# Kernel optimization log

Hardware: AMD Instinct MI355X
Metric: run time of the kernel (lower is better)

## Reference

```python
import jax, jax.numpy as jnp
import numpy as np

TEMPERATURE = 0.07
EPS = 1e-8

def setup_inputs() -> dict:
    key = jax.random.key(0)
    k1, k2 = jax.random.split(key)
    features = jax.random.normal(k1, (8192, 512), dtype=jnp.float32)
    labels = jax.random.randint(k2, (8192,), 0, 100, dtype=jnp.int64)
    return {"features": features, "labels": labels}

def reference(features, labels):
    # L2-normalize rows (torch F.normalize uses eps=1e-12 clamp on norm)
    norm = jnp.maximum(jnp.linalg.norm(features, axis=1, keepdims=True), 1e-12)
    f = features / norm                                   # [B, D]
    sim = jnp.matmul(f, f.T) / TEMPERATURE                # [B, B]
    B = features.shape[0]
    same_label = (labels[:, None] == labels[None, :]).astype(features.dtype)
    diag = jnp.eye(B, dtype=bool)
    mask = jnp.where(diag, 0.0, same_label)               # positives, diag removed
    exp_sim = jnp.where(diag, 0.0, jnp.exp(sim))          # diag zeroed
    positive_sum = jnp.sum(exp_sim * mask, axis=1)        # [B]
    negative_sum = jnp.sum(exp_sim * (1.0 - mask), axis=1)
    loss = -jnp.log(positive_sum / (positive_sum + negative_sum + EPS))
    return loss.mean()
```

## Files before the change

kernel.cpp:

```cpp
#include <hip/hip_runtime.h>

#define BATCH 8192
#define DIM   512
#define NBLK  1056

typedef __attribute__((ext_vector_type(2))) long long2_t;
typedef __attribute__((ext_vector_type(4))) float f32x4;
typedef unsigned short ushort_t;
typedef unsigned char  u8;

__device__ __forceinline__ void gload_lds16(const void* g, void* l){
  __builtin_amdgcn_global_load_lds(
      (const __attribute__((address_space(1))) void*)g,
      (__attribute__((address_space(3))) void*)l, 16, 0, 0);
}

template<int CTRL>
__device__ __forceinline__ float dpp_add(float v){
  int s = __builtin_amdgcn_update_dpp(0, __float_as_int(v), CTRL, 0xF, 0xF, true);
  return v + __int_as_float(s);
}
__device__ __forceinline__ float red16(float v){
  v = dpp_add<0xB1>(v);
  v = dpp_add<0x4E>(v);
  v = dpp_add<0x141>(v);
  v = dpp_add<0x140>(v);
  return v;
}

__device__ __forceinline__ u8 f2e4m3(float v){
  unsigned s = (__float_as_uint(v) >> 24) & 0x80u;
  float a = fabsf(v);
  if (a < 0.0009765625f) return (u8)s;
  if (a < 0.015625f){
    int q = (int)rintf(a * 512.0f);
    return (u8)(s | (unsigned)q);
  }
  unsigned u = __float_as_uint(a);
  int E = (int)(u >> 23) - 127;
  unsigned m = u & 0x7FFFFF;
  unsigned mant = m >> 20;
  unsigned rem  = m & 0xFFFFF;
  mant += (rem > 0x80000u || (rem == 0x80000u && (mant & 1u))) ? 1u : 0u;
  if (mant == 8u){ mant = 0u; E += 1; }
  return (u8)(s | ((unsigned)(E + 7) << 3) | mant);
}

__global__ __launch_bounds__(256) void k_normalize(const float* __restrict__ x,
                                                   u8* __restrict__ q){
  const int row  = blockIdx.x * 4 + (threadIdx.x >> 6);
  const int lane = threadIdx.x & 63;
  const float* xr = x + (size_t)row * DIM + lane * 8;
  float4 a = *(const float4*)xr;
  float4 b = *(const float4*)(xr + 4);
  float s = a.x*a.x + a.y*a.y + a.z*a.z + a.w*a.w
          + b.x*b.x + b.y*b.y + b.z*b.z + b.w*b.w;
  #pragma unroll
  for (int m = 1; m < 64; m <<= 1) s += __shfl_xor(s, m);
  const float inv = 1.0f / fmaxf(sqrtf(s), 1e-12f);
  float f[8] = {a.x, a.y, a.z, a.w, b.x, b.y, b.z, b.w};
  union { u8 b[8]; unsigned long long u; } pk;
  #pragma unroll
  for (int e = 0; e < 8; e++) pk.b[e] = f2e4m3(f[e] * inv);
  const int kb = lane >> 3;
  const int g  = lane & 7;
  const int sw = (row >> 1) & 3;
  const size_t off = (size_t)row * DIM + kb * 64
                   + (size_t)(((g & 3) ^ sw) * 16 + (g >> 2) * 8);
  *(unsigned long long*)(q + off) = pk.u;
}

__global__ __launch_bounds__(256, 2) void k_gemm(const u8* __restrict__ q,
                                                 const int* __restrict__ labels,
                                                 float* __restrict__ ppos,
                                                 float* __restrict__ ptot){
  __shared__ u8 sA[2][256 * 64];
  __shared__ u8 sB[2][128 * 64];
  __shared__ int labI[256], labJ[128];

  const int bid = (blockIdx.x & 7) * 132 + (blockIdx.x >> 3);
  int I = (int)((65.0f - sqrtf(4225.0f - 4.0f * (float)bid)) * 0.5f);
  while ((I + 1) * (64 - I) <= bid) I++;
  while (I * (65 - I) > bid) I--;
  const int J = 2 * I + (bid - I * (65 - I));
  const bool mirror = (J >= 2 * I + 2);
  const int rowbase = I * 256, colbase = J * 128;

  const int t    = threadIdx.x;
  const int lane = t & 63;
  const int w    = t >> 6;
  const int wr   = w >> 1, wc = w & 1;
  const int lrow = lane & 15;
  const int g    = lane >> 4;

  labI[t] = labels[rowbase + t];
  if (t < 128) labJ[t] = labels[colbase + t];

  const int gs = (g ^ ((lrow >> 1) & 3)) * 16;
  int ra[8], rb[4];
  #pragma unroll
  for (int m = 0; m < 8; m++) ra[m] = (wr * 128 + m * 16 + lrow) * 64 + gs;
  #pragma unroll
  for (int n = 0; n < 4; n++) rb[n] = (wc * 64 + n * 16 + lrow) * 64 + gs;

  const u8* srcA = q + (size_t)(rowbase + (t >> 2)) * DIM + (t & 3) * 16;
  const u8* srcB = q + (size_t)(colbase + (t >> 2)) * DIM + (t & 3) * 16;
  const int dL = t * 16;

#define STAGE(BUF, KT) do{                                                \
    gload_lds16(srcA + (KT) * 64,                  sA[BUF] + dL);         \
    gload_lds16(srcA + (KT) * 64 +  64 * DIM,      sA[BUF] + dL + 4096);  \
    gload_lds16(srcA + (KT) * 64 + 128 * DIM,      sA[BUF] + dL + 8192);  \
    gload_lds16(srcA + (KT) * 64 + 192 * DIM,      sA[BUF] + dL + 12288); \
    gload_lds16(srcB + (KT) * 64,                  sB[BUF] + dL);         \
    gload_lds16(srcB + (KT) * 64 +  64 * DIM,      sB[BUF] + dL + 4096);  \
  }while(0)

  f32x4 acc[8][4];
  #pragma unroll
  for (int m = 0; m < 8; m++)
    #pragma unroll
    for (int n = 0; n < 4; n++)
      acc[m][n] = (f32x4){0.f, 0.f, 0.f, 0.f};

  STAGE(0, 0);
  __syncthreads();

  for (int kt = 0; kt < 8; ++kt){
    const int cur = kt & 1;
    if (kt < 7) STAGE(cur ^ 1, kt + 1);
    const u8* pA = sA[cur];
    const u8* pB = sB[cur];
    long2_t av[8], bv[4];
    #pragma unroll
    for (int n = 0; n < 4; n++) bv[n] = *(const long2_t*)(pB + rb[n]);
    #pragma unroll
    for (int m = 0; m < 8; m++) av[m] = *(const long2_t*)(pA + ra[m]);
    #pragma unroll
    for (int m = 0; m < 8; m++)
      #pragma unroll
      for (int n = 0; n < 4; n++)
        acc[m][n] = __builtin_amdgcn_mfma_f32_16x16x32_fp8_fp8(
            av[m][0], bv[n][0], acc[m][n], 0, 0, 0);
    #pragma unroll
    for (int m = 0; m < 8; m++)
      #pragma unroll
      for (int n = 0; n < 4; n++)
        acc[m][n] = __builtin_amdgcn_mfma_f32_16x16x32_fp8_fp8(
            av[m][1], bv[n][1], acc[m][n], 0, 0, 0);
    __syncthreads();
  }
#undef STAGE

  const int i0 = rowbase + wr * 128;
  const int j0 = colbase + wc * 64;

  int li_[8][4], lj_[4];
  #pragma unroll
  for (int m = 0; m < 8; m++)
    #pragma unroll
    for (int e = 0; e < 4; e++)
      li_[m][e] = labI[wr * 128 + m * 16 + g * 4 + e];
  #pragma unroll
  for (int n = 0; n < 4; n++)
    lj_[n] = labJ[wc * 64 + n * 16 + lrow];

  const float invT = 14.285714285714286f;
  #pragma unroll
  for (int m = 0; m < 8; m++)
    #pragma unroll
    for (int n = 0; n < 4; n++)
      #pragma unroll
      for (int e = 0; e < 4; e++){
        int i = i0 + m * 16 + g * 4 + e;
        int j = j0 + n * 16 + lrow;
        acc[m][n][e] = (i == j) ? 0.0f : __expf(acc[m][n][e] * invT);
      }

  {
    float* pp = ppos + (size_t)(J * 2 + wc) * BATCH;
    float* pt = ptot + (size_t)(J * 2 + wc) * BATCH;
    #pragma unroll
    for (int m = 0; m < 8; m++){
      float tr[4] = {0, 0, 0, 0}, pr[4] = {0, 0, 0, 0};
      #pragma unroll
      for (int n = 0; n < 4; n++){
        int lj = lj_[n];
        #pragma unroll
        for (int e = 0; e < 4; e++){
          float v = acc[m][n][e];
          tr[e] += v;
          pr[e] += (li_[m][e] == lj) ? v : 0.0f;
        }
      }
      #pragma unroll
      for (int e = 0; e < 4; e++){
        tr[e] = red16(tr[e]);
        pr[e] = red16(pr[e]);
      }
      if (lrow == 0){
        int ib = i0 + m * 16 + g * 4;
        #pragma unroll
        for (int e = 0; e < 4; e++){
          pt[ib + e] = tr[e];
          pp[ib + e] = pr[e];
        }
      }
    }
  }

  if (mirror){
    #pragma unroll
    for (int h = 0; h < 2; h++){
      float* pp = ppos + (size_t)(I * 4 + wr * 2 + h) * BATCH;
      float* pt = ptot + (size_t)(I * 4 + wr * 2 + h) * BATCH;
      #pragma unroll
      for (int n = 0; n < 4; n++){
        float ts = 0.f, ps = 0.f;
        int lj = lj_[n];
        #pragma unroll
        for (int m = h * 4; m < h * 4 + 4; m++)
          #pragma unroll
          for (int e = 0; e < 4; e++){
            float v = acc[m][n][e];
            ts += v;
            ps += (li_[m][e] == lj) ? v : 0.0f;
          }
        ts += __shfl_xor(ts, 16); ps += __shfl_xor(ps, 16);
        ts += __shfl_xor(ts, 32); ps += __shfl_xor(ps, 32);
        if (lane < 16){
          int j = j0 + n * 16 + lane;
          pt[j] = ts;
          pp[j] = ps;
        }
      }
    }
  }
}

__global__ __launch_bounds__(256) void k_rowloss(const float* __restrict__ ppos,
                                                 const float* __restrict__ ptot,
                                                 float* __restrict__ bsum){
  __shared__ float sp[256], st2[256];
  const int t = threadIdx.x;
  const int r = blockIdx.x * 32 + (t & 31);
  const int c0 = t >> 5;
  float p = 0.f, tt = 0.f;
  for (int c = c0; c < 128; c += 8){
    p  += ppos[(size_t)c * BATCH + r];
    tt += ptot[(size_t)c * BATCH + r];
  }
  sp[t] = p; st2[t] = tt;
  __syncthreads();
  if (t < 32){
    float P = 0.f, T = 0.f;
    #pragma unroll
    for (int k = 0; k < 8; k++){ P += sp[t + k * 32]; T += st2[t + k * 32]; }
    sp[t] = -logf(P / (T + 1e-8f));
  }
  __syncthreads();
  if (t == 0){
    float s = 0.f;
    #pragma unroll
    for (int k = 0; k < 32; k++) s += sp[k];
    bsum[blockIdx.x] = s;
  }
}

__global__ __launch_bounds__(256) void k_final(const float* __restrict__ bsum,
                                               float* __restrict__ out){
  __shared__ float s4[4];
  float v = bsum[threadIdx.x];
  #pragma unroll
  for (int m = 1; m < 64; m <<= 1) v += __shfl_xor(v, m);
  if ((threadIdx.x & 63) == 0) s4[threadIdx.x >> 6] = v;
  __syncthreads();
  if (threadIdx.x == 0) out[0] = (s4[0] + s4[1] + s4[2] + s4[3]) * (1.0f / 8192.0f);
}

extern "C" void kernel_launch(void* const* d_in, const int* in_sizes, int n_in,
                              void* d_out, int out_size, void* d_ws, size_t ws_size,
                              hipStream_t stream){
  const float* x      = (const float*)d_in[0];
  const int*   labels = (const int*)d_in[1];
  float*       out    = (float*)d_out;

  char* ws = (char*)d_ws;
  u8*    q    = (u8*)ws;
  float* ppos = (float*)(ws + 8388608);
  float* ptot = (float*)(ws + 8388608 + 4194304);
  float* bsum = (float*)(ws + 8388608 + 8388608);

  k_normalize<<<BATCH / 4, 256, 0, stream>>>(x, q);
  k_gemm<<<NBLK, 256, 0, stream>>>(q, labels, ppos, ptot);
  k_rowloss<<<256, 256, 0, stream>>>(ppos, ptot, bsum);
  k_final<<<1, 256, 0, stream>>>(bsum, out);
}
```

Before: 59.55 us.

## Shrink GEMM tile to 128x128 over upper-triangular blocks with higher occupancy

Changes the symmetric Gram-matrix tiling from 256x128 tiles over a 2-column-wide triangular layout to square 128x128 tiles indexed over the upper triangle, giving 2080 blocks instead of 1056. Per-thread accumulators shrink from 8x4 to 4x4 MFMA tiles and LDS use drops, so launch bounds move to 3 blocks per CU. The aim is better load balance and occupancy across the CUs. In exchange, operand reuse per tile is lower, global/LDS traffic rises and more partial sums are written. It also passes a dynamic shared memory argument of 8192 bytes that the kernel does not appear to use.

```diff
diff --git a/kernel.cpp b/kernel.cpp
--- a/kernel.cpp
+++ b/kernel.cpp
@@ -2,12 +2,11 @@
 
 #define BATCH 8192
 #define DIM   512
-#define NBLK  1056
+#define NBLK  2080
 
 typedef __attribute__((ext_vector_type(2))) long long2_t;
 typedef __attribute__((ext_vector_type(4))) float f32x4;
-typedef unsigned short ushort_t;
-typedef unsigned char  u8;
+typedef unsigned char u8;
 
 __device__ __forceinline__ void gload_lds16(const void* g, void* l){
   __builtin_amdgcn_global_load_lds(
@@ -33,8 +32,8 @@
   float a = fabsf(v);
   if (a < 0.0009765625f) return (u8)s;
   if (a < 0.015625f){
-    int q = (int)rintf(a * 512.0f);
-    return (u8)(s | (unsigned)q);
+    int qd = (int)rintf(a * 512.0f);
+    return (u8)(s | (unsigned)qd);
   }
   unsigned u = __float_as_uint(a);
   int E = (int)(u >> 23) - 127;
@@ -70,21 +69,21 @@
   *(unsigned long long*)(q + off) = pk.u;
 }
 
-__global__ __launch_bounds__(256, 2) void k_gemm(const u8* __restrict__ q,
+__global__ __launch_bounds__(256, 3) void k_gemm(const u8* __restrict__ q,
                                                  const int* __restrict__ labels,
                                                  float* __restrict__ ppos,
                                                  float* __restrict__ ptot){
-  __shared__ u8 sA[2][256 * 64];
+  __shared__ u8 sA[2][128 * 64];
   __shared__ u8 sB[2][128 * 64];
-  __shared__ int labI[256], labJ[128];
-
-  const int bid = (blockIdx.x & 7) * 132 + (blockIdx.x >> 3);
-  int I = (int)((65.0f - sqrtf(4225.0f - 4.0f * (float)bid)) * 0.5f);
-  while ((I + 1) * (64 - I) <= bid) I++;
-  while (I * (65 - I) > bid) I--;
-  const int J = 2 * I + (bid - I * (65 - I));
-  const bool mirror = (J >= 2 * I + 2);
-  const int rowbase = I * 256, colbase = J * 128;
+  __shared__ int labI[128], labJ[128];
+
+  const int bid = (blockIdx.x & 7) * 260 + (blockIdx.x >> 3);
+  int bj = (int)((sqrtf(8.0f * (float)bid + 1.0f) - 1.0f) * 0.5f);
+  while ((bj + 1) * (bj + 2) / 2 <= bid) bj++;
+  while (bj * (bj + 1) / 2 > bid) bj--;
+  const int bi = bid - bj * (bj + 1) / 2;
+  const bool mirror = (bi != bj);
+  const int rowbase = bi * 128, colbase = bj * 128;
 
   const int t    = threadIdx.x;
   const int lane = t & 63;
@@ -93,13 +92,13 @@
   const int lrow = lane & 15;
   const int g    = lane >> 4;
 
-  labI[t] = labels[rowbase + t];
-  if (t < 128) labJ[t] = labels[colbase + t];
+  if (t < 128) labI[t] = labels[rowbase + t];
+  else         labJ[t - 128] = labels[colbase + (t - 128)];
 
   const int gs = (g ^ ((lrow >> 1) & 3)) * 16;
-  int ra[8], rb[4];
-  #pragma unroll
-  for (int m = 0; m < 8; m++) ra[m] = (wr * 128 + m * 16 + lrow) * 64 + gs;
+  int ra[4], rb[4];
+  #pragma unroll
+  for (int m = 0; m < 4; m++) ra[m] = (wr * 64 + m * 16 + lrow) * 64 + gs;
   #pragma unroll
   for (int n = 0; n < 4; n++) rb[n] = (wc * 64 + n * 16 + lrow) * 64 + gs;
 
@@ -108,17 +107,15 @@
   const int dL = t * 16;
 
 #define STAGE(BUF, KT) do{                                                \
-    gload_lds16(srcA + (KT) * 64,                  sA[BUF] + dL);         \
-    gload_lds16(srcA + (KT) * 64 +  64 * DIM,      sA[BUF] + dL + 4096);  \
-    gload_lds16(srcA + (KT) * 64 + 128 * DIM,      sA[BUF] + dL + 8192);  \
-    gload_lds16(srcA + (KT) * 64 + 192 * DIM,      sA[BUF] + dL + 12288); \
-    gload_lds16(srcB + (KT) * 64,                  sB[BUF] + dL);         \
-    gload_lds16(srcB + (KT) * 64 +  64 * DIM,      sB[BUF] + dL + 4096);  \
+    gload_lds16(srcA + (KT) * 64,             sA[BUF] + dL);              \
+    gload_lds16(srcA + (KT) * 64 + 64 * DIM,  sA[BUF] + dL + 4096);       \
+    gload_lds16(srcB + (KT) * 64,             sB[BUF] + dL);              \
+    gload_lds16(srcB + (KT) * 64 + 64 * DIM,  sB[BUF] + dL + 4096);       \
   }while(0)
 
-  f32x4 acc[8][4];
-  #pragma unroll
-  for (int m = 0; m < 8; m++)
+  f32x4 acc[4][4];
+  #pragma unroll
+  for (int m = 0; m < 4; m++)
     #pragma unroll
     for (int n = 0; n < 4; n++)
       acc[m][n] = (f32x4){0.f, 0.f, 0.f, 0.f};
@@ -131,19 +128,19 @@
     if (kt < 7) STAGE(cur ^ 1, kt + 1);
     const u8* pA = sA[cur];
     const u8* pB = sB[cur];
-    long2_t av[8], bv[4];
+    long2_t av[4], bv[4];
     #pragma unroll
     for (int n = 0; n < 4; n++) bv[n] = *(const long2_t*)(pB + rb[n]);
     #pragma unroll
-    for (int m = 0; m < 8; m++) av[m] = *(const long2_t*)(pA + ra[m]);
-    #pragma unroll
-    for (int m = 0; m < 8; m++)
+    for (int m = 0; m < 4; m++) av[m] = *(const long2_t*)(pA + ra[m]);
+    #pragma unroll
+    for (int m = 0; m < 4; m++)
       #pragma unroll
       for (int n = 0; n < 4; n++)
         acc[m][n] = __builtin_amdgcn_mfma_f32_16x16x32_fp8_fp8(
             av[m][0], bv[n][0], acc[m][n], 0, 0, 0);
     #pragma unroll
-    for (int m = 0; m < 8; m++)
+    for (int m = 0; m < 4; m++)
       #pragma unroll
       for (int n = 0; n < 4; n++)
         acc[m][n] = __builtin_amdgcn_mfma_f32_16x16x32_fp8_fp8(
@@ -152,22 +149,22 @@
   }
 #undef STAGE
 
-  const int i0 = rowbase + wr * 128;
+  const int i0 = rowbase + wr * 64;
   const int j0 = colbase + wc * 64;
 
-  int li_[8][4], lj_[4];
-  #pragma unroll
-  for (int m = 0; m < 8; m++)
+  int li_[4][4], lj_[4];
+  #pragma unroll
+  for (int m = 0; m < 4; m++)
     #pragma unroll
     for (int e = 0; e < 4; e++)
-      li_[m][e] = labI[wr * 128 + m * 16 + g * 4 + e];
+      li_[m][e] = labI[wr * 64 + m * 16 + g * 4 + e];
   #pragma unroll
   for (int n = 0; n < 4; n++)
     lj_[n] = labJ[wc * 64 + n * 16 + lrow];
 
   const float invT = 14.285714285714286f;
   #pragma unroll
-  for (int m = 0; m < 8; m++)
+  for (int m = 0; m < 4; m++)
     #pragma unroll
     for (int n = 0; n < 4; n++)
       #pragma unroll
@@ -178,10 +175,10 @@
       }
 
   {
-    float* pp = ppos + (size_t)(J * 2 + wc) * BATCH;
-    float* pt = ptot + (size_t)(J * 2 + wc) * BATCH;
-    #pragma unroll
-    for (int m = 0; m < 8; m++){
+    float* pp = ppos + (size_t)(2 * bj + wc) * BATCH;
+    float* pt = ptot + (size_t)(2 * bj + wc) * BATCH;
+    #pragma unroll
+    for (int m = 0; m < 4; m++){
       float tr[4] = {0, 0, 0, 0}, pr[4] = {0, 0, 0, 0};
       #pragma unroll
       for (int n = 0; n < 4; n++){
@@ -210,29 +207,26 @@
   }
 
   if (mirror){
-    #pragma unroll
-    for (int h = 0; h < 2; h++){
-      float* pp = ppos + (size_t)(I * 4 + wr * 2 + h) * BATCH;
-      float* pt = ptot + (size_t)(I * 4 + wr * 2 + h) * BATCH;
-      #pragma unroll
-      for (int n = 0; n < 4; n++){
-        float ts = 0.f, ps = 0.f;
-        int lj = lj_[n];
+    float* pp = ppos + (size_t)(2 * bi + wr) * BATCH;
+    float* pt = ptot + (size_t)(2 * bi + wr) * BATCH;
+    #pragma unroll
+    for (int n = 0; n < 4; n++){
+      float ts = 0.f, ps = 0.f;
+      int lj = lj_[n];
+      #pragma unroll
+      for (int m = 0; m < 4; m++)
         #pragma unroll
-        for (int m = h * 4; m < h * 4 + 4; m++)
-          #pragma unroll
-          for (int e = 0; e < 4; e++){
-            float v = acc[m][n][e];
-            ts += v;
-            ps += (li_[m][e] == lj) ? v : 0.0f;
-          }
-        ts += __shfl_xor(ts, 16); ps += __shfl_xor(ps, 16);
-        ts += __shfl_xor(ts, 32); ps += __shfl_xor(ps, 32);
-        if (lane < 16){
-          int j = j0 + n * 16 + lane;
-          pt[j] = ts;
-          pp[j] = ps;
+        for (int e = 0; e < 4; e++){
+          float v = acc[m][n][e];
+          ts += v;
+          ps += (li_[m][e] == lj) ? v : 0.0f;
         }
+      ts += __shfl_xor(ts, 16); ps += __shfl_xor(ps, 16);
+      ts += __shfl_xor(ts, 32); ps += __shfl_xor(ps, 32);
+      if (lane < 16){
+        int j = j0 + n * 16 + lane;
+        pt[j] = ts;
+        pp[j] = ps;
       }
     }
   }
@@ -292,7 +286,7 @@
   float* bsum = (float*)(ws + 8388608 + 8388608);
 
   k_normalize<<<BATCH / 4, 256, 0, stream>>>(x, q);
-  k_gemm<<<NBLK, 256, 0, stream>>>(q, labels, ppos, ptot);
+  k_gemm<<<NBLK, 256, 8192, stream>>>(q, labels, ppos, ptot);
   k_rowloss<<<256, 256, 0, stream>>>(ppos, ptot, bsum);
   k_final<<<1, 256, 0, stream>>>(bsum, out);
 }
```

Result: faster. 56.15 us (-5.7%).
